# Kernel tuning notes

Hardware: AMD Instinct MI355X
Metric: run time of the kernel (lower is better)

Reference implementation:

```python
import jax, jax.numpy as jnp
import numpy as np
from jax import lax

WINDOW = 9
LOSS_WEIGHT = 1.0
EPS = 1e-05
BALANCE = 0.2

_DN = ('NCHW', 'OIHW', 'NCHW')

def _local_sum(x, k=WINDOW):
    # Separable box-filter sum == conv2d with ones((1,1,k,k)), padding=k//2.
    pad = k // 2
    kh = jnp.ones((1, 1, k, 1), x.dtype)
    kw = jnp.ones((1, 1, 1, k), x.dtype)
    y = lax.conv_general_dilated(x, kh, (1, 1), [(pad, pad), (0, 0)], dimension_numbers=_DN)
    return lax.conv_general_dilated(y, kw, (1, 1), [(0, 0), (pad, pad)], dimension_numbers=_DN)

def _lncc_loss(pred, target, k=WINDOW, eps=EPS):
    n = k * k
    pred_mean = _local_sum(pred, k) / n
    target_mean = _local_sum(target, k) / n
    # NOTE: faithful to source: variance uses raw local sum of squares minus mean^2
    pred_var = jnp.clip(_local_sum(pred * pred, k) - pred_mean * pred_mean, 0.0, None)
    target_var = jnp.clip(_local_sum(target * target, k) - target_mean * target_mean, 0.0, None)
    cov = _local_sum(pred * target, k) - pred_mean * target_mean
    lncc = cov / (jnp.sqrt(pred_var + eps) * jnp.sqrt(target_var + eps))
    return 1.0 - jnp.mean(lncc)

def setup_inputs() -> dict:
    key = jax.random.key(0)
    k1, k2, k3 = jax.random.split(key, 3)
    B, H, W = 16, 512, 512
    pred = jax.random.normal(k1, (B, 1, H, W), dtype=jnp.float32)
    target = jax.random.normal(k2, (B, 1, H, W), dtype=jnp.float32)
    mask = jax.random.normal(k3, (B, 2, H, W), dtype=jnp.float32)
    return {"pred": pred, "target": target, "mask": mask}

def reference(pred, target, mask):
    m = jnp.argmax(mask, axis=1)[:, None].astype(pred.dtype)  # [B,1,H,W]
    p_pred1 = (1.0 - m) * pred
    p_pred2 = (1.0 - m) * target
    n_pred1 = m * pred
    n_pred2 = m * target
    return LOSS_WEIGHT * (BALANCE * _lncc_loss(p_pred1, p_pred2)
                          - (1.0 - BALANCE) * _lncc_loss(n_pred1, n_pred2))
```

## Files before the change

### kernel.cpp

```cpp
#include <hip/hip_runtime.h>

#define NB   16
#define NH   512
#define NW   512
#define RAD  4
#define PADW (NW + 2*RAD)
#define BH   8
#define TX   128
#define BANDS 2
#define NTHREADS 256
#define STRIPES (NH / (BH * BANDS))
#define NBLOCKS (NB * STRIPES)
#define EPSF 1e-5f

__device__ __forceinline__ float lncc_val(float Sa, float Sb, float Saa, float Sbb, float Sab) {
    const float inv_n = 1.0f / 81.0f;
    float ma  = Sa * inv_n;
    float mb  = Sb * inv_n;
    float va  = fmaxf(Saa - ma * ma, 0.0f);
    float vb  = fmaxf(Sbb - mb * mb, 0.0f);
    float cov = Sab - ma * mb;
    return cov * rsqrtf((va + EPSF) * (vb + EPSF));
}

__global__ __launch_bounds__(NTHREADS, 2)
void lncc_main(const float* __restrict__ pred,
               const float* __restrict__ targ,
               const float* __restrict__ mask,
               float* __restrict__ part)
{
    __shared__ float LV[BANDS][10][PADW];
    __shared__ float wred[8];

    const int tid  = threadIdx.x;
    const int tx   = tid & (TX - 1);
    const int ty   = tid >> 7;
    const int col0 = tx * 4;

    const int b  = blockIdx.x / STRIPES;
    const int s  = blockIdx.x % STRIPES;
    const int y0 = (s * BANDS + ty) * BH;

    {
        float* lf = &LV[0][0][0];
        for (int i = tid; i < BANDS * 10 * PADW; i += NTHREADS) lf[i] = 0.0f;
    }
    __syncthreads();

    const size_t hw   = (size_t)NH * NW;
    const float* prow = pred + (size_t)b * hw;
    const float* trow = targ + (size_t)b * hw;
    const float* mrow = mask + (size_t)b * 2 * hw;

    float V[10][4];
    #pragma unroll
    for (int q = 0; q < 10; ++q) {
        #pragma unroll
        for (int c = 0; c < 4; ++c) V[q][c] = 0.0f;
    }

    auto accum = [&](int y, float sgn) {
        size_t off = (size_t)y * NW + col0;
        float4 pv = *reinterpret_cast<const float4*>(prow + off);
        float4 tv = *reinterpret_cast<const float4*>(trow + off);
        float4 m0 = *reinterpret_cast<const float4*>(mrow + off);
        float4 m1 = *reinterpret_cast<const float4*>(mrow + off + hw);
        float pa[4] = {pv.x, pv.y, pv.z, pv.w};
        float ta[4] = {tv.x, tv.y, tv.z, tv.w};
        float c0[4] = {m0.x, m0.y, m0.z, m0.w};
        float c1[4] = {m1.x, m1.y, m1.z, m1.w};
        #pragma unroll
        for (int c = 0; c < 4; ++c) {
            float p  = pa[c], t = ta[c];
            float mm = (c1[c] > c0[c]) ? sgn : 0.0f;
            float pp = p * p, tt = t * t, pt = p * t;
            V[0][c] += sgn * p;  V[1][c] += sgn * t;
            V[2][c] += sgn * pp; V[3][c] += sgn * tt; V[4][c] += sgn * pt;
            V[5][c] += mm * p;   V[6][c] += mm * t;
            V[7][c] += mm * pp;  V[8][c] += mm * tt;  V[9][c] += mm * pt;
        }
    };

    #pragma unroll
    for (int j = -RAD; j < RAD; ++j) {
        int y = y0 + j;
        if (y >= 0 && y < NH) accum(y, 1.0f);
    }

    float sum_p = 0.0f, sum_n = 0.0f;

    for (int r = 0; r < BH; ++r) {
        int y  = y0 + r;
        int ye = y + RAD;
        if (ye < NH) accum(ye, 1.0f);

        #pragma unroll
        for (int q = 0; q < 10; ++q) {
            float4 v = make_float4(V[q][0], V[q][1], V[q][2], V[q][3]);
            *reinterpret_cast<float4*>(&LV[ty][q][RAD + col0]) = v;
        }
        __syncthreads();

        float Hh[10][4];
        #pragma unroll
        for (int q = 0; q < 10; ++q) {
            float4 a  = *reinterpret_cast<const float4*>(&LV[ty][q][col0]);
            float4 bq = *reinterpret_cast<const float4*>(&LV[ty][q][col0 + 4]);
            float4 cq = *reinterpret_cast<const float4*>(&LV[ty][q][col0 + 8]);
            float w0=a.x,  w1=a.y,  w2=a.z,  w3=a.w;
            float w4=bq.x, w5=bq.y, w6=bq.z, w7=bq.w;
            float w8=cq.x, w9=cq.y, w10=cq.z, w11=cq.w;
            float h = ((w0+w1)+(w2+w3)) + ((w4+w5)+(w6+w7)) + w8;
            Hh[q][0] = h;
            h += w9  - w0; Hh[q][1] = h;
            h += w10 - w1; Hh[q][2] = h;
            h += w11 - w2; Hh[q][3] = h;
        }
        __syncthreads();

        #pragma unroll
        for (int c = 0; c < 4; ++c) {
            float Sa=Hh[0][c], Sb=Hh[1][c], Saa=Hh[2][c], Sbb=Hh[3][c], Sab=Hh[4][c];
            float Ma=Hh[5][c], Mb=Hh[6][c], Maa=Hh[7][c], Mbb=Hh[8][c], Mab=Hh[9][c];
            sum_n += lncc_val(Ma, Mb, Maa, Mbb, Mab);
            sum_p += lncc_val(Sa - Ma, Sb - Mb, Saa - Maa, Sbb - Mbb, Sab - Mab);
        }

        if (r < BH - 1) {
            int yl = y - RAD;
            if (yl >= 0) accum(yl, -1.0f);
        }
    }

    #pragma unroll
    for (int off = 32; off > 0; off >>= 1) {
        sum_p += __shfl_down(sum_p, off, 64);
        sum_n += __shfl_down(sum_n, off, 64);
    }
    int wave = tid >> 6, lane = tid & 63;
    if (lane == 0) { wred[wave] = sum_p; wred[4 + wave] = sum_n; }
    __syncthreads();
    if (tid == 0) {
        float sp = wred[0] + wred[1] + wred[2] + wred[3];
        float sn = wred[4] + wred[5] + wred[6] + wred[7];
        part[blockIdx.x]           = sp;
        part[NBLOCKS + blockIdx.x] = sn;
    }
}

__global__ void lncc_finalize(const float* __restrict__ part, float* __restrict__ out) {
    __shared__ float w[8];
    int tid = threadIdx.x;
    float sp = 0.0f, sn = 0.0f;
    for (int i = tid; i < NBLOCKS; i += 256) {
        sp += part[i];
        sn += part[NBLOCKS + i];
    }
    #pragma unroll
    for (int off = 32; off > 0; off >>= 1) {
        sp += __shfl_down(sp, off, 64);
        sn += __shfl_down(sn, off, 64);
    }
    int wave = tid >> 6, lane = tid & 63;
    if (lane == 0) { w[wave] = sp; w[4 + wave] = sn; }
    __syncthreads();
    if (tid == 0) {
        double SP = (double)w[0] + (double)w[1] + (double)w[2] + (double)w[3];
        double SN = (double)w[4] + (double)w[5] + (double)w[6] + (double)w[7];
        const double npix = (double)NB * (double)NH * (double)NW;
        double mp = SP / npix;
        double mn = SN / npix;
        out[0] = (float)(0.2 * (1.0 - mp) - 0.8 * (1.0 - mn));
    }
}

extern "C" void kernel_launch(void* const* d_in, const int* in_sizes, int n_in,
                              void* d_out, int out_size, void* d_ws, size_t ws_size,
                              hipStream_t stream) {
    const float* pred = (const float*)d_in[0];
    const float* targ = (const float*)d_in[1];
    const float* mask = (const float*)d_in[2];
    float* part = (float*)d_ws;

    lncc_main<<<dim3(NBLOCKS), dim3(NTHREADS), 0, stream>>>(pred, targ, mask, part);
    lncc_finalize<<<dim3(1), dim3(256), 0, stream>>>(part, (float*)d_out);
}
```

Measured before the change: 117.1 us.

## Replace shared-memory horizontal box sum with single-wave register shuffles

Each block is now one 64-lane wave that covers a full 512-pixel row band, with each lane holding 8 columns. The horizontal 9-tap sum is built from neighbour-lane shuffles instead of a shared-memory staging buffer. This removes both per-row __syncthreads barriers and the LDS traffic. In exchange it doubles per-thread register state (80 accumulators), which may lower occupancy, and it launches many small one-wave blocks.

```diff
diff --git a/kernel.cpp b/kernel.cpp
--- a/kernel.cpp
+++ b/kernel.cpp
@@ -4,13 +4,9 @@
 #define NH   512
 #define NW   512
 #define RAD  4
-#define PADW (NW + 2*RAD)
 #define BH   8
-#define TX   128
-#define BANDS 2
-#define NTHREADS 256
-#define STRIPES (NH / (BH * BANDS))
-#define NBLOCKS (NB * STRIPES)
+#define NBANDS (NH / BH)
+#define NBLOCKS (NB * NBANDS)
 #define EPSF 1e-5f
 
 __device__ __forceinline__ float lncc_val(float Sa, float Sb, float Saa, float Sbb, float Sab) {
@@ -23,68 +19,73 @@
     return cov * rsqrtf((va + EPSF) * (vb + EPSF));
 }
 
-__global__ __launch_bounds__(NTHREADS, 2)
+template<int SGN>
+__device__ __forceinline__ void accum_row(const float* __restrict__ prow,
+                                          const float* __restrict__ trow,
+                                          const float* __restrict__ mrow,
+                                          size_t hw, int y, int col0,
+                                          float (&V)[10][8])
+{
+    size_t off = (size_t)y * NW + col0;
+    float4 p0 = *reinterpret_cast<const float4*>(prow + off);
+    float4 p1 = *reinterpret_cast<const float4*>(prow + off + 4);
+    float4 t0 = *reinterpret_cast<const float4*>(trow + off);
+    float4 t1 = *reinterpret_cast<const float4*>(trow + off + 4);
+    float4 a0 = *reinterpret_cast<const float4*>(mrow + off);
+    float4 a1 = *reinterpret_cast<const float4*>(mrow + off + 4);
+    float4 b0 = *reinterpret_cast<const float4*>(mrow + off + hw);
+    float4 b1 = *reinterpret_cast<const float4*>(mrow + off + hw + 4);
+
+    float p[8]  = {p0.x,p0.y,p0.z,p0.w, p1.x,p1.y,p1.z,p1.w};
+    float t[8]  = {t0.x,t0.y,t0.z,t0.w, t1.x,t1.y,t1.z,t1.w};
+    float c0[8] = {a0.x,a0.y,a0.z,a0.w, a1.x,a1.y,a1.z,a1.w};
+    float c1[8] = {b0.x,b0.y,b0.z,b0.w, b1.x,b1.y,b1.z,b1.w};
+
+    #pragma unroll
+    for (int c = 0; c < 8; ++c) {
+        float pv = p[c], tv = t[c];
+        float s  = (c1[c] > c0[c]) ? 1.0f : 0.0f;
+        float pp = pv * pv, tt = tv * tv, pt = pv * tv;
+        if (SGN > 0) {
+            V[0][c] += pv; V[1][c] += tv; V[2][c] += pp; V[3][c] += tt; V[4][c] += pt;
+            V[5][c] = fmaf(s, pv, V[5][c]); V[6][c] = fmaf(s, tv, V[6][c]);
+            V[7][c] = fmaf(s, pp, V[7][c]); V[8][c] = fmaf(s, tt, V[8][c]);
+            V[9][c] = fmaf(s, pt, V[9][c]);
+        } else {
+            V[0][c] -= pv; V[1][c] -= tv; V[2][c] -= pp; V[3][c] -= tt; V[4][c] -= pt;
+            V[5][c] = fmaf(-s, pv, V[5][c]); V[6][c] = fmaf(-s, tv, V[6][c]);
+            V[7][c] = fmaf(-s, pp, V[7][c]); V[8][c] = fmaf(-s, tt, V[8][c]);
+            V[9][c] = fmaf(-s, pt, V[9][c]);
+        }
+    }
+}
+
+__global__ __launch_bounds__(64)
 void lncc_main(const float* __restrict__ pred,
                const float* __restrict__ targ,
                const float* __restrict__ mask,
                float* __restrict__ part)
 {
-    __shared__ float LV[BANDS][10][PADW];
-    __shared__ float wred[8];
-
-    const int tid  = threadIdx.x;
-    const int tx   = tid & (TX - 1);
-    const int ty   = tid >> 7;
-    const int col0 = tx * 4;
-
-    const int b  = blockIdx.x / STRIPES;
-    const int s  = blockIdx.x % STRIPES;
-    const int y0 = (s * BANDS + ty) * BH;
-
-    {
-        float* lf = &LV[0][0][0];
-        for (int i = tid; i < BANDS * 10 * PADW; i += NTHREADS) lf[i] = 0.0f;
-    }
-    __syncthreads();
+    const int lane = threadIdx.x;
+    const int col0 = lane * 8;
+    const int b    = blockIdx.x / NBANDS;
+    const int y0   = (blockIdx.x % NBANDS) * BH;
 
     const size_t hw   = (size_t)NH * NW;
     const float* prow = pred + (size_t)b * hw;
     const float* trow = targ + (size_t)b * hw;
     const float* mrow = mask + (size_t)b * 2 * hw;
 
-    float V[10][4];
-    #pragma unroll
-    for (int q = 0; q < 10; ++q) {
+    float V[10][8];
+    #pragma unroll
+    for (int q = 0; q < 10; ++q)
         #pragma unroll
-        for (int c = 0; c < 4; ++c) V[q][c] = 0.0f;
-    }
-
-    auto accum = [&](int y, float sgn) {
-        size_t off = (size_t)y * NW + col0;
-        float4 pv = *reinterpret_cast<const float4*>(prow + off);
-        float4 tv = *reinterpret_cast<const float4*>(trow + off);
-        float4 m0 = *reinterpret_cast<const float4*>(mrow + off);
-        float4 m1 = *reinterpret_cast<const float4*>(mrow + off + hw);
-        float pa[4] = {pv.x, pv.y, pv.z, pv.w};
-        float ta[4] = {tv.x, tv.y, tv.z, tv.w};
-        float c0[4] = {m0.x, m0.y, m0.z, m0.w};
-        float c1[4] = {m1.x, m1.y, m1.z, m1.w};
-        #pragma unroll
-        for (int c = 0; c < 4; ++c) {
-            float p  = pa[c], t = ta[c];
-            float mm = (c1[c] > c0[c]) ? sgn : 0.0f;
-            float pp = p * p, tt = t * t, pt = p * t;
-            V[0][c] += sgn * p;  V[1][c] += sgn * t;
-            V[2][c] += sgn * pp; V[3][c] += sgn * tt; V[4][c] += sgn * pt;
-            V[5][c] += mm * p;   V[6][c] += mm * t;
-            V[7][c] += mm * pp;  V[8][c] += mm * tt;  V[9][c] += mm * pt;
-        }
-    };
+        for (int c = 0; c < 8; ++c) V[q][c] = 0.0f;
 
     #pragma unroll
     for (int j = -RAD; j < RAD; ++j) {
         int y = y0 + j;
-        if (y >= 0 && y < NH) accum(y, 1.0f);
+        if (y >= 0) accum_row<1>(prow, trow, mrow, hw, y, col0, V);
     }
 
     float sum_p = 0.0f, sum_n = 0.0f;
@@ -92,43 +93,67 @@
     for (int r = 0; r < BH; ++r) {
         int y  = y0 + r;
         int ye = y + RAD;
-        if (ye < NH) accum(ye, 1.0f);
-
-        #pragma unroll
-        for (int q = 0; q < 10; ++q) {
-            float4 v = make_float4(V[q][0], V[q][1], V[q][2], V[q][3]);
-            *reinterpret_cast<float4*>(&LV[ty][q][RAD + col0]) = v;
-        }
-        __syncthreads();
-
-        float Hh[10][4];
-        #pragma unroll
-        for (int q = 0; q < 10; ++q) {
-            float4 a  = *reinterpret_cast<const float4*>(&LV[ty][q][col0]);
-            float4 bq = *reinterpret_cast<const float4*>(&LV[ty][q][col0 + 4]);
-            float4 cq = *reinterpret_cast<const float4*>(&LV[ty][q][col0 + 8]);
-            float w0=a.x,  w1=a.y,  w2=a.z,  w3=a.w;
-            float w4=bq.x, w5=bq.y, w6=bq.z, w7=bq.w;
-            float w8=cq.x, w9=cq.y, w10=cq.z, w11=cq.w;
-            float h = ((w0+w1)+(w2+w3)) + ((w4+w5)+(w6+w7)) + w8;
-            Hh[q][0] = h;
-            h += w9  - w0; Hh[q][1] = h;
-            h += w10 - w1; Hh[q][2] = h;
-            h += w11 - w2; Hh[q][3] = h;
-        }
-        __syncthreads();
-
-        #pragma unroll
-        for (int c = 0; c < 4; ++c) {
-            float Sa=Hh[0][c], Sb=Hh[1][c], Saa=Hh[2][c], Sbb=Hh[3][c], Sab=Hh[4][c];
-            float Ma=Hh[5][c], Mb=Hh[6][c], Maa=Hh[7][c], Mbb=Hh[8][c], Mab=Hh[9][c];
-            sum_n += lncc_val(Ma, Mb, Maa, Mbb, Mab);
-            sum_p += lncc_val(Sa - Ma, Sb - Mb, Saa - Maa, Sbb - Mbb, Sab - Mab);
+        if (ye < NH) accum_row<1>(prow, trow, mrow, hw, ye, col0, V);
+
+        {
+            float HhA[10][4];
+            #pragma unroll
+            for (int q = 0; q < 10; ++q) {
+                float hp0 = __shfl_up(V[q][4], 1);
+                float hp1 = __shfl_up(V[q][5], 1);
+                float hp2 = __shfl_up(V[q][6], 1);
+                float hp3 = __shfl_up(V[q][7], 1);
+                hp0 = (lane > 0) ? hp0 : 0.0f;
+                hp1 = (lane > 0) ? hp1 : 0.0f;
+                hp2 = (lane > 0) ? hp2 : 0.0f;
+                hp3 = (lane > 0) ? hp3 : 0.0f;
+                float h = ((hp0 + hp1) + (hp2 + hp3))
+                        + ((V[q][0] + V[q][1]) + (V[q][2] + V[q][3])) + V[q][4];
+                HhA[q][0] = h;
+                h += V[q][5] - hp0; HhA[q][1] = h;
+                h += V[q][6] - hp1; HhA[q][2] = h;
+                h += V[q][7] - hp2; HhA[q][3] = h;
+            }
+            #pragma unroll
+            for (int c = 0; c < 4; ++c) {
+                float Sa=HhA[0][c], Sb=HhA[1][c], Saa=HhA[2][c], Sbb=HhA[3][c], Sab=HhA[4][c];
+                float Ma=HhA[5][c], Mb=HhA[6][c], Maa=HhA[7][c], Mbb=HhA[8][c], Mab=HhA[9][c];
+                sum_n += lncc_val(Ma, Mb, Maa, Mbb, Mab);
+                sum_p += lncc_val(Sa-Ma, Sb-Mb, Saa-Maa, Sbb-Mbb, Sab-Mab);
+            }
+        }
+
+        {
+            float HhB[10][4];
+            #pragma unroll
+            for (int q = 0; q < 10; ++q) {
+                float hn0 = __shfl_down(V[q][0], 1);
+                float hn1 = __shfl_down(V[q][1], 1);
+                float hn2 = __shfl_down(V[q][2], 1);
+                float hn3 = __shfl_down(V[q][3], 1);
+                hn0 = (lane < 63) ? hn0 : 0.0f;
+                hn1 = (lane < 63) ? hn1 : 0.0f;
+                hn2 = (lane < 63) ? hn2 : 0.0f;
+                hn3 = (lane < 63) ? hn3 : 0.0f;
+                float h = ((V[q][0] + V[q][1]) + (V[q][2] + V[q][3]))
+                        + ((V[q][4] + V[q][5]) + (V[q][6] + V[q][7])) + hn0;
+                HhB[q][0] = h;
+                h += hn1 - V[q][0]; HhB[q][1] = h;
+                h += hn2 - V[q][1]; HhB[q][2] = h;
+                h += hn3 - V[q][2]; HhB[q][3] = h;
+            }
+            #pragma unroll
+            for (int c = 0; c < 4; ++c) {
+                float Sa=HhB[0][c], Sb=HhB[1][c], Saa=HhB[2][c], Sbb=HhB[3][c], Sab=HhB[4][c];
+                float Ma=HhB[5][c], Mb=HhB[6][c], Maa=HhB[7][c], Mbb=HhB[8][c], Mab=HhB[9][c];
+                sum_n += lncc_val(Ma, Mb, Maa, Mbb, Mab);
+                sum_p += lncc_val(Sa-Ma, Sb-Mb, Saa-Maa, Sbb-Mbb, Sab-Mab);
+            }
         }
 
         if (r < BH - 1) {
             int yl = y - RAD;
-            if (yl >= 0) accum(yl, -1.0f);
+            if (yl >= 0) accum_row<-1>(prow, trow, mrow, hw, yl, col0, V);
         }
     }
 
@@ -137,14 +162,9 @@
         sum_p += __shfl_down(sum_p, off, 64);
         sum_n += __shfl_down(sum_n, off, 64);
     }
-    int wave = tid >> 6, lane = tid & 63;
-    if (lane == 0) { wred[wave] = sum_p; wred[4 + wave] = sum_n; }
-    __syncthreads();
-    if (tid == 0) {
-        float sp = wred[0] + wred[1] + wred[2] + wred[3];
-        float sn = wred[4] + wred[5] + wred[6] + wred[7];
-        part[blockIdx.x]           = sp;
-        part[NBLOCKS + blockIdx.x] = sn;
+    if (lane == 0) {
+        part[blockIdx.x]           = sum_p;
+        part[NBLOCKS + blockIdx.x] = sum_n;
     }
 }
 
@@ -182,6 +202,6 @@
     const float* mask = (const float*)d_in[2];
     float* part = (float*)d_ws;
 
-    lncc_main<<<dim3(NBLOCKS), dim3(NTHREADS), 0, stream>>>(pred, targ, mask, part);
+    lncc_main<<<dim3(NBLOCKS), dim3(64), 0, stream>>>(pred, targ, mask, part);
     lncc_finalize<<<dim3(1), dim3(256), 0, stream>>>(part, (float*)d_out);
 }
```

Measured after the change: 117.6 us. About the same (+0.5%).
